# Kernel tuning notes

Measured on AMD Instinct MI355X. Metric: run time of the kernel, lower is better.

Reference implementation:

```python
import jax, jax.numpy as jnp
import numpy as np

D_MODEL = 1024
HIDDEN = 2048            # hidden_dimension // num_smaller_experts_per_expert
E_ROUTED = 14            # total_num_experts*num_smaller - num_shared
E_SHARED = 2
TOP_K = 2                # num_activated*num_smaller - num_shared
EPS = 1e-9               # config.epsilon
RMS_EPS = 1.1920929e-07  # torch RMSNorm default eps=None -> finfo(float32).eps


def setup_inputs() -> dict:
    key = jax.random.key(0)
    ks = jax.random.split(key, 9)
    B, T = 2, 1024
    x = jax.random.normal(ks[0], (B, T, D_MODEL), dtype=jnp.float32)
    router_w = jax.random.normal(ks[1], (D_MODEL, E_ROUTED), dtype=jnp.float32) * 0.006
    rms_w = jnp.ones((E_ROUTED, D_MODEL), dtype=jnp.float32)
    w1 = jax.random.normal(ks[2], (E_ROUTED, D_MODEL, HIDDEN), dtype=jnp.float32) * 0.02
    w2 = jax.random.normal(ks[3], (E_ROUTED, HIDDEN, D_MODEL), dtype=jnp.float32) * 0.02
    rms_w_s = jnp.ones((E_SHARED, D_MODEL), dtype=jnp.float32)
    w1_s = jax.random.normal(ks[4], (E_SHARED, D_MODEL, HIDDEN), dtype=jnp.float32) * 0.02
    w2_s = jax.random.normal(ks[5], (E_SHARED, HIDDEN, D_MODEL), dtype=jnp.float32) * 0.02
    return {"x": x, "router_w": router_w, "rms_w": rms_w, "w1": w1, "w2": w2,
            "rms_w_s": rms_w_s, "w1_s": w1_s, "w2_s": w2_s}


def _ffn(xn, rw, W1, W2):
    # RMSNorm -> Linear -> SiLU -> Linear (dropout is identity in eval)
    ms = jnp.mean(xn * xn, axis=-1, keepdims=True)
    h = (xn * jax.lax.rsqrt(ms + RMS_EPS)) * rw
    return jax.nn.silu(h @ W1) @ W2


def reference(x, router_w, rms_w, w1, w2, rms_w_s, w1_s, w2_s):
    B, T, D = x.shape
    N = B * T
    xf = x.reshape(N, D)
    # router gates + top-k sparsification + renormalization
    gates = jax.nn.softmax(xf @ router_w, axis=-1)          # [N, E]
    top_v, top_i = jax.lax.top_k(gates, TOP_K)              # [N, K]
    masked = jnp.zeros_like(gates).at[jnp.arange(N)[:, None], top_i].set(top_v)
    masked = masked / (masked.sum(axis=-1, keepdims=True) + EPS)  # [N, E]
    # routed experts: compute each expert on all tokens, combine with sparse gate weights
    # (same math as dispatch/index_add combine since masked is 0 off the top-k)
    routed = jax.vmap(lambda rw_, W1_, W2_: _ffn(xf, rw_, W1_, W2_))(rms_w, w1, w2)  # [E, N, D]
    routed_out = jnp.einsum('end,ne->nd', routed, masked)
    # shared experts: unweighted sum
    shared = jax.vmap(lambda rw_, W1_, W2_: _ffn(xf, rw_, W1_, W2_))(rms_w_s, w1_s, w2_s).sum(0)
    return (routed_out + shared).reshape(B, T, D)
```

## Files before the change

kernel.cpp:

```cpp
#include <hip/hip_runtime.h>
#include <hip/hip_bf16.h>
#include <cstdint>
#include <cstddef>

#define D_MODEL 1024
#define HIDDEN 2048
#define E_ROUTED 14
#define E_TOT 16
#define NTOK 2048
#define NASSIGN 4096
#define NROWS 8192

typedef __bf16 bf16x8 __attribute__((ext_vector_type(8)));
typedef float f32x4 __attribute__((ext_vector_type(4)));

static __device__ __forceinline__ unsigned short f2b(float f) {
  unsigned int u = __builtin_bit_cast(unsigned int, f);
  u += 0x7fffu + ((u >> 16) & 1u);
  return (unsigned short)(u >> 16);
}

#define ASYNC_COPY16(gptr, lptr)                                                        \
  __builtin_amdgcn_global_load_lds(                                                     \
      (const __attribute__((address_space(1))) unsigned int*)(gptr),                    \
      (__attribute__((address_space(3))) unsigned int*)(lptr), 16, 0, 0)

__global__ __launch_bounds__(256) void router_kernel(
    const float* __restrict__ x, const float* __restrict__ rweight,
    int* __restrict__ topi, float* __restrict__ topw,
    unsigned short* __restrict__ xhat) {
  int n = blockIdx.x, tid = threadIdx.x;
  const float4 xv = reinterpret_cast<const float4*>(x + (size_t)n * D_MODEL)[tid];
  float ss = xv.x * xv.x + xv.y * xv.y + xv.z * xv.z + xv.w * xv.w;
  float lg[E_ROUTED];
#pragma unroll
  for (int e = 0; e < E_ROUTED; ++e) lg[e] = 0.f;
  const float xa[4] = {xv.x, xv.y, xv.z, xv.w};
#pragma unroll
  for (int i = 0; i < 4; ++i) {
    const float* rw = rweight + (size_t)(tid * 4 + i) * E_ROUTED;
    float xd = xa[i];
#pragma unroll
    for (int e = 0; e < E_ROUTED; ++e) lg[e] = fmaf(xd, rw[e], lg[e]);
  }
#pragma unroll
  for (int off = 32; off > 0; off >>= 1) {
    ss += __shfl_xor(ss, off);
#pragma unroll
    for (int e = 0; e < E_ROUTED; ++e) lg[e] += __shfl_xor(lg[e], off);
  }
  __shared__ float red[4][16];
  int wid = tid >> 6, lane = tid & 63;
  if (lane == 0) {
    red[wid][0] = ss;
#pragma unroll
    for (int e = 0; e < E_ROUTED; ++e) red[wid][1 + e] = lg[e];
  }
  __syncthreads();
  __shared__ float s_scale;
  if (tid == 0) {
    float fin[15];
    for (int v = 0; v < 15; ++v) fin[v] = red[0][v] + red[1][v] + red[2][v] + red[3][v];
    s_scale = rsqrtf(fin[0] * (1.f / D_MODEL) + 1.1920929e-07f);
    float mx = fin[1];
    for (int e = 1; e < E_ROUTED; ++e) mx = fmaxf(mx, fin[1 + e]);
    float p[E_ROUTED]; float Z = 0.f;
    for (int e = 0; e < E_ROUTED; ++e) { p[e] = __expf(fin[1 + e] - mx); Z += p[e]; }
    int i0 = 0; float v0 = p[0];
    for (int e = 1; e < E_ROUTED; ++e) if (p[e] > v0) { v0 = p[e]; i0 = e; }
    int i1 = (i0 == 0) ? 1 : 0; float v1 = p[i1];
    for (int e = 0; e < E_ROUTED; ++e) if (e != i0 && p[e] > v1) { v1 = p[e]; i1 = e; }
    v0 /= Z; v1 /= Z;
    float inv = 1.f / (v0 + v1 + 1e-9f);
    topi[2 * n] = i0; topi[2 * n + 1] = i1;
    topw[2 * n] = v0 * inv; topw[2 * n + 1] = v1 * inv;
  }
  __syncthreads();
  float sc = s_scale;
  ushort4 hx;
  hx.x = f2b(xv.x * sc); hx.y = f2b(xv.y * sc);
  hx.z = f2b(xv.z * sc); hx.w = f2b(xv.w * sc);
  reinterpret_cast<ushort4*>(xhat + (size_t)n * D_MODEL)[tid] = hx;
}

__global__ __launch_bounds__(256) void count_kernel(const int* __restrict__ topi,
                                                    int* __restrict__ goff,
                                                    int* __restrict__ cursor) {
  __shared__ int cnt[E_ROUTED];
  int tid = threadIdx.x;
  if (tid < E_ROUTED) cnt[tid] = 0;
  __syncthreads();
  for (int i = tid; i < NASSIGN; i += 256) atomicAdd(&cnt[topi[i]], 1);
  __syncthreads();
  if (tid == 0) {
    int acc = 0;
    for (int e = 0; e < E_ROUTED; ++e) { goff[e] = acc; cursor[e] = acc; acc += cnt[e]; }
    goff[E_ROUTED] = acc;
  }
}

__global__ __launch_bounds__(256) void scatter_kernel(
    const int* __restrict__ topi, const float* __restrict__ topw,
    int* __restrict__ cursor, int* __restrict__ row_token,
    float* __restrict__ row_gate, int* __restrict__ token_rows) {
  int i = blockIdx.x * 256 + threadIdx.x;
  if (i >= NASSIGN) return;
  int e = topi[i];
  int pos = atomicAdd(&cursor[e], 1);
  row_token[pos] = i >> 1;
  row_gate[pos] = topw[i];
  token_rows[i] = pos;
}

template <int K, int N, bool SCALE>
__global__ __launch_bounds__(256) void convT_kernel(
    const float* __restrict__ Wr, const float* __restrict__ Ws,
    const float* __restrict__ RWr, const float* __restrict__ RWs,
    unsigned short* __restrict__ outT) {
  __shared__ float tile[64][65];
  int g = blockIdx.z;
  const float* src = (g < E_ROUTED) ? Wr + (size_t)g * K * N
                                    : Ws + (size_t)(g - E_ROUTED) * K * N;
  const float* rw = nullptr;
  if constexpr (SCALE)
    rw = (g < E_ROUTED) ? RWr + (size_t)g * K : RWs + (size_t)(g - E_ROUTED) * K;
  int k0 = blockIdx.y * 64, nn0 = blockIdx.x * 64;
  int t = threadIdx.x;
  int kk = t >> 4, nc = (t & 15) * 4;
#pragma unroll
  for (int j = 0; j < 4; ++j) {
    int k = kk + j * 16;
    float4 v = *(const float4*)(src + (size_t)(k0 + k) * N + nn0 + nc);
    float s = 1.f;
    if constexpr (SCALE) s = rw[k0 + k];
    tile[k][nc]     = v.x * s;
    tile[k][nc + 1] = v.y * s;
    tile[k][nc + 2] = v.z * s;
    tile[k][nc + 3] = v.w * s;
  }
  __syncthreads();
  int k8 = (t & 7) * 8;
#pragma unroll
  for (int p = 0; p < 2; ++p) {
    int n = (t >> 3) + p * 32;
    uint4 pk;
    pk.x = (unsigned)f2b(tile[k8 + 0][n]) | ((unsigned)f2b(tile[k8 + 1][n]) << 16);
    pk.y = (unsigned)f2b(tile[k8 + 2][n]) | ((unsigned)f2b(tile[k8 + 3][n]) << 16);
    pk.z = (unsigned)f2b(tile[k8 + 4][n]) | ((unsigned)f2b(tile[k8 + 5][n]) << 16);
    pk.w = (unsigned)f2b(tile[k8 + 6][n]) | ((unsigned)f2b(tile[k8 + 7][n]) << 16);
    *(uint4*)(outT + ((size_t)g * N + nn0 + n) * K + k0 + k8) = pk;
  }
}

template <bool G1, int KTOT, int NTOT>
__global__ __launch_bounds__(256, 3) void ffn_gemm(
    const int* __restrict__ goff, const int* __restrict__ row_token,
    const float* __restrict__ row_gate,
    const unsigned short* __restrict__ Abase,
    const unsigned short* __restrict__ Wt,
    unsigned short* __restrict__ Hout, float* __restrict__ Yout) {
  int g = blockIdx.z;
  int grpStart, cnt;
  if (g < E_ROUTED) { grpStart = goff[g]; cnt = goff[g + 1] - goff[g]; }
  else { grpStart = NASSIGN + (g - E_ROUTED) * NTOK; cnt = NTOK; }
  int m0 = blockIdx.y * 128;
  if (m0 >= cnt) return;
  int n0 = blockIdx.x * 128;

  __shared__ __align__(16) char smem[32 * 1024];
  char* sA = smem;
  char* sB = smem + 16 * 1024;

  int tid = threadIdx.x, lane = tid & 63, wid = tid >> 6;
  int wr = (wid >> 1) * 64, wc = (wid & 1) * 64;
  int lrow = lane >> 3;
  int swz = lrow << 4;
  int colB = ((lane & 7) << 4) ^ swz;

  const char* aSrc[4];
  const char* bSrc[4];
#pragma unroll
  for (int i = 0; i < 4; ++i) {
    int row = wid * 32 + i * 8 + lrow;
    int rIdx = m0 + row; if (rIdx >= cnt) rIdx = cnt - 1;
    int srcRow;
    if constexpr (G1) srcRow = (g < E_ROUTED) ? row_token[grpStart + rIdx] : rIdx;
    else srcRow = grpStart + rIdx;
    aSrc[i] = (const char*)(Abase + (size_t)srcRow * KTOT) + colB;
    bSrc[i] = (const char*)(Wt + ((size_t)g * NTOT + n0 + row) * KTOT) + colB;
  }

  f32x4 acc[4][4];
#pragma unroll
  for (int m = 0; m < 4; ++m)
#pragma unroll
    for (int n = 0; n < 4; ++n)
#pragma unroll
      for (int c = 0; c < 4; ++c) acc[m][n][c] = 0.f;

  for (int kt = 0; kt < KTOT / 64; ++kt) {
#pragma unroll
    for (int i = 0; i < 4; ++i) ASYNC_COPY16(aSrc[i], sA + wid * 4096 + i * 1024);
#pragma unroll
    for (int i = 0; i < 4; ++i) ASYNC_COPY16(bSrc[i], sB + wid * 4096 + i * 1024);
#pragma unroll
    for (int i = 0; i < 4; ++i) { aSrc[i] += 128; bSrc[i] += 128; }
    __syncthreads();

#pragma unroll
    for (int ks = 0; ks < 2; ++ks) {
      int kb = ks * 64 + ((lane >> 4) << 4);
      bf16x8 af[4], bfr[4];
#pragma unroll
      for (int m = 0; m < 4; ++m) {
        int r = wr + m * 16 + (lane & 15);
        af[m] = *(const bf16x8*)(sA + (r << 7) + (kb ^ ((r & 7) << 4)));
      }
#pragma unroll
      for (int n = 0; n < 4; ++n) {
        int r = wc + n * 16 + (lane & 15);
        bfr[n] = *(const bf16x8*)(sB + (r << 7) + (kb ^ ((r & 7) << 4)));
      }
#pragma unroll
      for (int m = 0; m < 4; ++m)
#pragma unroll
        for (int n = 0; n < 4; ++n)
          acc[m][n] = __builtin_amdgcn_mfma_f32_16x16x32_bf16(af[m], bfr[n], acc[m][n], 0, 0, 0);
    }
    __syncthreads();
  }

  int lr = (lane >> 4) * 4, lc = lane & 15;
#pragma unroll
  for (int m = 0; m < 4; ++m) {
    int rloc = m0 + wr + m * 16 + lr;
#pragma unroll
    for (int j = 0; j < 4; ++j) {
      if (rloc + j < cnt) {
        size_t r = (size_t)(grpStart + rloc + j);
        if constexpr (G1) {
#pragma unroll
          for (int n = 0; n < 4; ++n) {
            float v = acc[m][n][j];
            float sv = v / (1.f + __expf(-v));
            Hout[r * HIDDEN + (n0 + wc + n * 16 + lc)] = f2b(sv);
          }
        } else {
          float gate = 1.f;
          if (g < E_ROUTED) gate = row_gate[r];
#pragma unroll
          for (int n = 0; n < 4; ++n)
            Yout[r * D_MODEL + (n0 + wc + n * 16 + lc)] = acc[m][n][j] * gate;
        }
      }
    }
  }
}

__global__ __launch_bounds__(256) void combine_kernel(
    const float* __restrict__ y, const int* __restrict__ token_rows,
    float* __restrict__ out) {
  int n = blockIdx.x, tid = threadIdx.x;
  int a0 = token_rows[2 * n], a1 = token_rows[2 * n + 1];
  const float4* y0 = reinterpret_cast<const float4*>(y + (size_t)a0 * D_MODEL);
  const float4* y1 = reinterpret_cast<const float4*>(y + (size_t)a1 * D_MODEL);
  const float4* s0 = reinterpret_cast<const float4*>(y + (size_t)(NASSIGN + n) * D_MODEL);
  const float4* s1 = reinterpret_cast<const float4*>(y + (size_t)(NASSIGN + NTOK + n) * D_MODEL);
  float4 a = y0[tid], b = y1[tid], c = s0[tid], d = s1[tid];
  float4 r;
  r.x = a.x + b.x + c.x + d.x;
  r.y = a.y + b.y + c.y + d.y;
  r.z = a.z + b.z + c.z + d.z;
  r.w = a.w + b.w + c.w + d.w;
  reinterpret_cast<float4*>(out + (size_t)n * D_MODEL)[tid] = r;
}

extern "C" void kernel_launch(void* const* d_in, const int* in_sizes, int n_in,
                              void* d_out, int out_size, void* d_ws, size_t ws_size,
                              hipStream_t stream) {
  const float* x        = (const float*)d_in[0];
  const float* router_w = (const float*)d_in[1];
  const float* rms_w    = (const float*)d_in[2];
  const float* w1       = (const float*)d_in[3];
  const float* w2       = (const float*)d_in[4];
  const float* rms_w_s  = (const float*)d_in[5];
  const float* w1_s     = (const float*)d_in[6];
  const float* w2_s     = (const float*)d_in[7];
  float* out = (float*)d_out;

  char* ws = (char*)d_ws;
  unsigned short* xhat = (unsigned short*)ws;
  unsigned short* h    = (unsigned short*)(ws + ((size_t)4 << 20));
  float* y             = (float*)(ws + ((size_t)36 << 20));
  unsigned short* w1t  = (unsigned short*)(ws + ((size_t)68 << 20));
  unsigned short* w2t  = (unsigned short*)(ws + ((size_t)132 << 20));
  char* meta = ws + ((size_t)196 << 20);
  int*   topi       = (int*)(meta);
  float* topw       = (float*)(meta + (16 << 10));
  int*   row_token  = (int*)(meta + (32 << 10));
  float* row_gate   = (float*)(meta + (48 << 10));
  int*   token_rows = (int*)(meta + (64 << 10));
  int*   goff       = (int*)(meta + (80 << 10));
  int*   cursor     = (int*)(meta + (80 << 10) + 256);

  router_kernel<<<NTOK, 256, 0, stream>>>(x, router_w, topi, topw, xhat);
  count_kernel<<<1, 256, 0, stream>>>(topi, goff, cursor);
  scatter_kernel<<<NASSIGN / 256, 256, 0, stream>>>(topi, topw, cursor, row_token,
                                                    row_gate, token_rows);
  convT_kernel<D_MODEL, HIDDEN, true><<<dim3(HIDDEN / 64, D_MODEL / 64, E_TOT), 256, 0, stream>>>(
      w1, w1_s, rms_w, rms_w_s, w1t);
  convT_kernel<HIDDEN, D_MODEL, false><<<dim3(D_MODEL / 64, HIDDEN / 64, E_TOT), 256, 0, stream>>>(
      w2, w2_s, nullptr, nullptr, w2t);
  ffn_gemm<true, D_MODEL, HIDDEN><<<dim3(HIDDEN / 128, 16, E_TOT), 256, 0, stream>>>(
      goff, row_token, row_gate, xhat, w1t, h, nullptr);
  ffn_gemm<false, HIDDEN, D_MODEL><<<dim3(D_MODEL / 128, 16, E_TOT), 256, 0, stream>>>(
      goff, row_token, row_gate, h, w2t, nullptr, y);
  combine_kernel<<<NTOK, 256, 0, stream>>>(y, token_rows, out);
}
```

Baseline: 241.9 us.

## Merge weight transpose kernels and remap GEMM workgroups across XCDs

Merges the two weight convert/transpose launches into one kernel over a flat 16384-block grid, saving one launch and its tail. In the FFN GEMMs, the block index is remapped so consecutive tiles go to the same XCD (stride-8 interleave), aiming for better L2 reuse of weight and activation tiles. The remap makes early exit depend on the permuted row index, so blocks with no work are spread differently across the grid.

```diff
diff --git a/kernel.cpp b/kernel.cpp
--- a/kernel.cpp
+++ b/kernel.cpp
@@ -113,19 +113,10 @@
 }
 
 template <int K, int N, bool SCALE>
-__global__ __launch_bounds__(256) void convT_kernel(
-    const float* __restrict__ Wr, const float* __restrict__ Ws,
-    const float* __restrict__ RWr, const float* __restrict__ RWs,
-    unsigned short* __restrict__ outT) {
-  __shared__ float tile[64][65];
-  int g = blockIdx.z;
-  const float* src = (g < E_ROUTED) ? Wr + (size_t)g * K * N
-                                    : Ws + (size_t)(g - E_ROUTED) * K * N;
-  const float* rw = nullptr;
-  if constexpr (SCALE)
-    rw = (g < E_ROUTED) ? RWr + (size_t)g * K : RWs + (size_t)(g - E_ROUTED) * K;
-  int k0 = blockIdx.y * 64, nn0 = blockIdx.x * 64;
-  int t = threadIdx.x;
+static __device__ __forceinline__ void convT_body(
+    const float* __restrict__ src, const float* __restrict__ rw,
+    unsigned short* __restrict__ outT, float (*tile)[65],
+    int k0, int nn0, int t) {
   int kk = t >> 4, nc = (t & 15) * 4;
 #pragma unroll
   for (int j = 0; j < 4; ++j) {
@@ -148,7 +139,35 @@
     pk.y = (unsigned)f2b(tile[k8 + 2][n]) | ((unsigned)f2b(tile[k8 + 3][n]) << 16);
     pk.z = (unsigned)f2b(tile[k8 + 4][n]) | ((unsigned)f2b(tile[k8 + 5][n]) << 16);
     pk.w = (unsigned)f2b(tile[k8 + 6][n]) | ((unsigned)f2b(tile[k8 + 7][n]) << 16);
-    *(uint4*)(outT + ((size_t)g * N + nn0 + n) * K + k0 + k8) = pk;
+    *(uint4*)(outT + ((size_t)(nn0 + n)) * K + k0 + k8) = pk;
+  }
+}
+
+__global__ __launch_bounds__(256) void convT_both(
+    const float* __restrict__ w1, const float* __restrict__ w1_s,
+    const float* __restrict__ rms_w, const float* __restrict__ rms_w_s,
+    const float* __restrict__ w2, const float* __restrict__ w2_s,
+    unsigned short* __restrict__ w1t, unsigned short* __restrict__ w2t) {
+  __shared__ float tile[64][65];
+  int id = blockIdx.x, t = threadIdx.x;
+  constexpr int TPE1 = (HIDDEN / 64) * (D_MODEL / 64);
+  if (id < TPE1 * E_TOT) {
+    int g = id >> 9, tt = id & 511;
+    int nn0 = (tt & 31) * 64, k0 = (tt >> 5) * 64;
+    const float* src = (g < E_ROUTED) ? w1 + (size_t)g * D_MODEL * HIDDEN
+                                      : w1_s + (size_t)(g - E_ROUTED) * D_MODEL * HIDDEN;
+    const float* rw = (g < E_ROUTED) ? rms_w + (size_t)g * D_MODEL
+                                     : rms_w_s + (size_t)(g - E_ROUTED) * D_MODEL;
+    convT_body<D_MODEL, HIDDEN, true>(src, rw, w1t + (size_t)g * HIDDEN * D_MODEL,
+                                      tile, k0, nn0, t);
+  } else {
+    id -= TPE1 * E_TOT;
+    int g = id >> 9, tt = id & 511;
+    int nn0 = (tt & 15) * 64, k0 = (tt >> 4) * 64;
+    const float* src = (g < E_ROUTED) ? w2 + (size_t)g * HIDDEN * D_MODEL
+                                      : w2_s + (size_t)(g - E_ROUTED) * HIDDEN * D_MODEL;
+    convT_body<HIDDEN, D_MODEL, false>(src, nullptr, w2t + (size_t)g * D_MODEL * HIDDEN,
+                                       tile, k0, nn0, t);
   }
 }
 
@@ -163,94 +182,105 @@
   int grpStart, cnt;
   if (g < E_ROUTED) { grpStart = goff[g]; cnt = goff[g + 1] - goff[g]; }
   else { grpStart = NASSIGN + (g - E_ROUTED) * NTOK; cnt = NTOK; }
-  int m0 = blockIdx.y * 128;
-  if (m0 >= cnt) return;
-  int n0 = blockIdx.x * 128;
-
-  __shared__ __align__(16) char smem[32 * 1024];
-  char* sA = smem;
-  char* sB = smem + 16 * 1024;
-
-  int tid = threadIdx.x, lane = tid & 63, wid = tid >> 6;
-  int wr = (wid >> 1) * 64, wc = (wid & 1) * 64;
-  int lrow = lane >> 3;
-  int swz = lrow << 4;
-  int colB = ((lane & 7) << 4) ^ swz;
-
-  const char* aSrc[4];
-  const char* bSrc[4];
-#pragma unroll
-  for (int i = 0; i < 4; ++i) {
-    int row = wid * 32 + i * 8 + lrow;
-    int rIdx = m0 + row; if (rIdx >= cnt) rIdx = cnt - 1;
-    int srcRow;
-    if constexpr (G1) srcRow = (g < E_ROUTED) ? row_token[grpStart + rIdx] : rIdx;
-    else srcRow = grpStart + rIdx;
-    aSrc[i] = (const char*)(Abase + (size_t)srcRow * KTOT) + colB;
-    bSrc[i] = (const char*)(Wt + ((size_t)g * NTOT + n0 + row) * KTOT) + colB;
-  }
-
-  f32x4 acc[4][4];
-#pragma unroll
-  for (int m = 0; m < 4; ++m)
-#pragma unroll
-    for (int n = 0; n < 4; ++n)
-#pragma unroll
-      for (int c = 0; c < 4; ++c) acc[m][n][c] = 0.f;
-
-  for (int kt = 0; kt < KTOT / 64; ++kt) {
-#pragma unroll
-    for (int i = 0; i < 4; ++i) ASYNC_COPY16(aSrc[i], sA + wid * 4096 + i * 1024);
-#pragma unroll
-    for (int i = 0; i < 4; ++i) ASYNC_COPY16(bSrc[i], sB + wid * 4096 + i * 1024);
-#pragma unroll
-    for (int i = 0; i < 4; ++i) { aSrc[i] += 128; bSrc[i] += 128; }
-    __syncthreads();
-
-#pragma unroll
-    for (int ks = 0; ks < 2; ++ks) {
-      int kb = ks * 64 + ((lane >> 4) << 4);
-      bf16x8 af[4], bfr[4];
-#pragma unroll
-      for (int m = 0; m < 4; ++m) {
-        int r = wr + m * 16 + (lane & 15);
-        af[m] = *(const bf16x8*)(sA + (r << 7) + (kb ^ ((r & 7) << 4)));
+
+  {
+    int NX = gridDim.x, NY = gridDim.y;
+    int nwg = NX * NY;
+    int d = blockIdx.y * NX + blockIdx.x;
+    int cpx = nwg >> 3;
+    int w = (d & 7) * cpx + (d >> 3);
+    int myb = w % NY;
+    int nxb = w / NY;
+    if (myb * 128 >= cnt) return;
+    g = g;
+    int m0 = myb * 128;
+    int n0 = nxb * 128;
+
+    __shared__ __align__(16) char smem[32 * 1024];
+    char* sA = smem;
+    char* sB = smem + 16 * 1024;
+
+    int tid = threadIdx.x, lane = tid & 63, wid = tid >> 6;
+    int wr = (wid >> 1) * 64, wc = (wid & 1) * 64;
+    int lrow = lane >> 3;
+    int swz = lrow << 4;
+    int colB = ((lane & 7) << 4) ^ swz;
+
+    const char* aSrc[4];
+    const char* bSrc[4];
+#pragma unroll
+    for (int i = 0; i < 4; ++i) {
+      int row = wid * 32 + i * 8 + lrow;
+      int rIdx = m0 + row; if (rIdx >= cnt) rIdx = cnt - 1;
+      int srcRow;
+      if constexpr (G1) srcRow = (g < E_ROUTED) ? row_token[grpStart + rIdx] : rIdx;
+      else srcRow = grpStart + rIdx;
+      aSrc[i] = (const char*)(Abase + (size_t)srcRow * KTOT) + colB;
+      bSrc[i] = (const char*)(Wt + ((size_t)g * NTOT + n0 + row) * KTOT) + colB;
+    }
+
+    f32x4 acc[4][4];
+#pragma unroll
+    for (int m = 0; m < 4; ++m)
+#pragma unroll
+      for (int n = 0; n < 4; ++n)
+#pragma unroll
+        for (int c = 0; c < 4; ++c) acc[m][n][c] = 0.f;
+
+    for (int kt = 0; kt < KTOT / 64; ++kt) {
+#pragma unroll
+      for (int i = 0; i < 4; ++i) ASYNC_COPY16(aSrc[i], sA + wid * 4096 + i * 1024);
+#pragma unroll
+      for (int i = 0; i < 4; ++i) ASYNC_COPY16(bSrc[i], sB + wid * 4096 + i * 1024);
+#pragma unroll
+      for (int i = 0; i < 4; ++i) { aSrc[i] += 128; bSrc[i] += 128; }
+      __syncthreads();
+
+#pragma unroll
+      for (int ks = 0; ks < 2; ++ks) {
+        int kb = ks * 64 + ((lane >> 4) << 4);
+        bf16x8 af[4], bfr[4];
+#pragma unroll
+        for (int m = 0; m < 4; ++m) {
+          int r = wr + m * 16 + (lane & 15);
+          af[m] = *(const bf16x8*)(sA + (r << 7) + (kb ^ ((r & 7) << 4)));
+        }
+#pragma unroll
+        for (int n = 0; n < 4; ++n) {
+          int r = wc + n * 16 + (lane & 15);
+          bfr[n] = *(const bf16x8*)(sB + (r << 7) + (kb ^ ((r & 7) << 4)));
+        }
+#pragma unroll
+        for (int m = 0; m < 4; ++m)
+#pragma unroll
+          for (int n = 0; n < 4; ++n)
+            acc[m][n] = __builtin_amdgcn_mfma_f32_16x16x32_bf16(af[m], bfr[n], acc[m][n], 0, 0, 0);
       }
-#pragma unroll
-      for (int n = 0; n < 4; ++n) {
-        int r = wc + n * 16 + (lane & 15);
-        bfr[n] = *(const bf16x8*)(sB + (r << 7) + (kb ^ ((r & 7) << 4)));
-      }
-#pragma unroll
-      for (int m = 0; m < 4; ++m)
-#pragma unroll
-        for (int n = 0; n < 4; ++n)
-          acc[m][n] = __builtin_amdgcn_mfma_f32_16x16x32_bf16(af[m], bfr[n], acc[m][n], 0, 0, 0);
+      __syncthreads();
     }
-    __syncthreads();
-  }
-
-  int lr = (lane >> 4) * 4, lc = lane & 15;
-#pragma unroll
-  for (int m = 0; m < 4; ++m) {
-    int rloc = m0 + wr + m * 16 + lr;
-#pragma unroll
-    for (int j = 0; j < 4; ++j) {
-      if (rloc + j < cnt) {
-        size_t r = (size_t)(grpStart + rloc + j);
-        if constexpr (G1) {
-#pragma unroll
-          for (int n = 0; n < 4; ++n) {
-            float v = acc[m][n][j];
-            float sv = v / (1.f + __expf(-v));
-            Hout[r * HIDDEN + (n0 + wc + n * 16 + lc)] = f2b(sv);
+
+    int lr = (lane >> 4) * 4, lc = lane & 15;
+#pragma unroll
+    for (int m = 0; m < 4; ++m) {
+      int rloc = m0 + wr + m * 16 + lr;
+#pragma unroll
+      for (int j = 0; j < 4; ++j) {
+        if (rloc + j < cnt) {
+          size_t r = (size_t)(grpStart + rloc + j);
+          if constexpr (G1) {
+#pragma unroll
+            for (int n = 0; n < 4; ++n) {
+              float v = acc[m][n][j];
+              float sv = v / (1.f + __expf(-v));
+              Hout[r * HIDDEN + (n0 + wc + n * 16 + lc)] = f2b(sv);
+            }
+          } else {
+            float gate = 1.f;
+            if (g < E_ROUTED) gate = row_gate[r];
+#pragma unroll
+            for (int n = 0; n < 4; ++n)
+              Yout[r * D_MODEL + (n0 + wc + n * 16 + lc)] = acc[m][n][j] * gate;
           }
-        } else {
-          float gate = 1.f;
-          if (g < E_ROUTED) gate = row_gate[r];
-#pragma unroll
-          for (int n = 0; n < 4; ++n)
-            Yout[r * D_MODEL + (n0 + wc + n * 16 + lc)] = acc[m][n][j] * gate;
         }
       }
     }
@@ -284,8 +314,8 @@
   const float* w1       = (const float*)d_in[3];
   const float* w2       = (const float*)d_in[4];
   const float* rms_w_s  = (const float*)d_in[5];
-  const float* w1_s     = (const float*)d_in[6];
-  const float* w2_s     = (const float*)d_in[7];
+  const float* w1_s    = (const float*)d_in[6];
+  const float* w2_s    = (const float*)d_in[7];
   float* out = (float*)d_out;
 
   char* ws = (char*)d_ws;
@@ -307,10 +337,7 @@
   count_kernel<<<1, 256, 0, stream>>>(topi, goff, cursor);
   scatter_kernel<<<NASSIGN / 256, 256, 0, stream>>>(topi, topw, cursor, row_token,
                                                     row_gate, token_rows);
-  convT_kernel<D_MODEL, HIDDEN, true><<<dim3(HIDDEN / 64, D_MODEL / 64, E_TOT), 256, 0, stream>>>(
-      w1, w1_s, rms_w, rms_w_s, w1t);
-  convT_kernel<HIDDEN, D_MODEL, false><<<dim3(D_MODEL / 64, HIDDEN / 64, E_TOT), 256, 0, stream>>>(
-      w2, w2_s, nullptr, nullptr, w2t);
+  convT_both<<<16384, 256, 0, stream>>>(w1, w1_s, rms_w, rms_w_s, w2, w2_s, w1t, w2t);
   ffn_gemm<true, D_MODEL, HIDDEN><<<dim3(HIDDEN / 128, 16, E_TOT), 256, 0, stream>>>(
       goff, row_token, row_gate, xhat, w1t, h, nullptr);
   ffn_gemm<false, HIDDEN, D_MODEL><<<dim3(D_MODEL / 128, 16, E_TOT), 256, 0, stream>>>(
```

Result: no change. 242.2 us (+0.1%).

## Widen weight transpose tiles with bf16 LDS staging and remap GEMM blocks across XCDs

Applied to the files above, without the earlier changes.

The weight transpose-convert kernel now processes 64x256 tiles, converts to bf16 before staging in shared memory, and has each thread write a full 128-byte contiguous output row segment. This is meant to cut LDS traffic and improve write coalescing in the weight-prep pass, which moves large volumes of fp32 weights. Separately, the FFN GEMM remaps its block index so that blocks are distributed across the 8 XCDs, with neighbouring tiles on the same XCD to share L2. The remapping assumes the tile count is divisible by 8 and adds a little index arithmetic. The new LDS reads are 2-byte column reads with possible bank conflicts.

```diff
diff --git a/kernel.cpp b/kernel.cpp
--- a/kernel.cpp
+++ b/kernel.cpp
@@ -117,38 +117,38 @@
     const float* __restrict__ Wr, const float* __restrict__ Ws,
     const float* __restrict__ RWr, const float* __restrict__ RWs,
     unsigned short* __restrict__ outT) {
-  __shared__ float tile[64][65];
+  __shared__ unsigned short tile[64][256];
   int g = blockIdx.z;
   const float* src = (g < E_ROUTED) ? Wr + (size_t)g * K * N
                                     : Ws + (size_t)(g - E_ROUTED) * K * N;
   const float* rw = nullptr;
   if constexpr (SCALE)
     rw = (g < E_ROUTED) ? RWr + (size_t)g * K : RWs + (size_t)(g - E_ROUTED) * K;
-  int k0 = blockIdx.y * 64, nn0 = blockIdx.x * 64;
-  int t = threadIdx.x;
-  int kk = t >> 4, nc = (t & 15) * 4;
-#pragma unroll
-  for (int j = 0; j < 4; ++j) {
-    int k = kk + j * 16;
-    float4 v = *(const float4*)(src + (size_t)(k0 + k) * N + nn0 + nc);
+  int k0 = blockIdx.y * 64, n0 = blockIdx.x * 256;
+  int t = threadIdx.x, w = t >> 6, l = t & 63;
+
+#pragma unroll
+  for (int r = 0; r < 16; ++r) {
+    int row = r * 4 + w;
+    float4 v = *(const float4*)(src + (size_t)(k0 + row) * N + n0 + l * 4);
     float s = 1.f;
-    if constexpr (SCALE) s = rw[k0 + k];
-    tile[k][nc]     = v.x * s;
-    tile[k][nc + 1] = v.y * s;
-    tile[k][nc + 2] = v.z * s;
-    tile[k][nc + 3] = v.w * s;
-  }
-  __syncthreads();
-  int k8 = (t & 7) * 8;
-#pragma unroll
-  for (int p = 0; p < 2; ++p) {
-    int n = (t >> 3) + p * 32;
-    uint4 pk;
-    pk.x = (unsigned)f2b(tile[k8 + 0][n]) | ((unsigned)f2b(tile[k8 + 1][n]) << 16);
-    pk.y = (unsigned)f2b(tile[k8 + 2][n]) | ((unsigned)f2b(tile[k8 + 3][n]) << 16);
-    pk.z = (unsigned)f2b(tile[k8 + 4][n]) | ((unsigned)f2b(tile[k8 + 5][n]) << 16);
-    pk.w = (unsigned)f2b(tile[k8 + 6][n]) | ((unsigned)f2b(tile[k8 + 7][n]) << 16);
-    *(uint4*)(outT + ((size_t)g * N + nn0 + n) * K + k0 + k8) = pk;
+    if constexpr (SCALE) s = rw[k0 + row];
+    ushort4 b;
+    b.x = f2b(v.x * s); b.y = f2b(v.y * s);
+    b.z = f2b(v.z * s); b.w = f2b(v.w * s);
+    *(ushort4*)(&tile[row][l * 4]) = b;
+  }
+  __syncthreads();
+
+  unsigned short* dst = outT + ((size_t)g * N + n0 + t) * K + k0;
+#pragma unroll
+  for (int c = 0; c < 8; ++c) {
+    unsigned int u0 = (unsigned int)tile[c * 8 + 0][t] | ((unsigned int)tile[c * 8 + 1][t] << 16);
+    unsigned int u1 = (unsigned int)tile[c * 8 + 2][t] | ((unsigned int)tile[c * 8 + 3][t] << 16);
+    unsigned int u2 = (unsigned int)tile[c * 8 + 4][t] | ((unsigned int)tile[c * 8 + 5][t] << 16);
+    unsigned int u3 = (unsigned int)tile[c * 8 + 6][t] | ((unsigned int)tile[c * 8 + 7][t] << 16);
+    uint4 pk = {u0, u1, u2, u3};
+    *(uint4*)(dst + c * 8) = pk;
   }
 }
 
@@ -163,94 +163,104 @@
   int grpStart, cnt;
   if (g < E_ROUTED) { grpStart = goff[g]; cnt = goff[g + 1] - goff[g]; }
   else { grpStart = NASSIGN + (g - E_ROUTED) * NTOK; cnt = NTOK; }
-  int m0 = blockIdx.y * 128;
-  if (m0 >= cnt) return;
-  int n0 = blockIdx.x * 128;
-
-  __shared__ __align__(16) char smem[32 * 1024];
-  char* sA = smem;
-  char* sB = smem + 16 * 1024;
-
-  int tid = threadIdx.x, lane = tid & 63, wid = tid >> 6;
-  int wr = (wid >> 1) * 64, wc = (wid & 1) * 64;
-  int lrow = lane >> 3;
-  int swz = lrow << 4;
-  int colB = ((lane & 7) << 4) ^ swz;
-
-  const char* aSrc[4];
-  const char* bSrc[4];
-#pragma unroll
-  for (int i = 0; i < 4; ++i) {
-    int row = wid * 32 + i * 8 + lrow;
-    int rIdx = m0 + row; if (rIdx >= cnt) rIdx = cnt - 1;
-    int srcRow;
-    if constexpr (G1) srcRow = (g < E_ROUTED) ? row_token[grpStart + rIdx] : rIdx;
-    else srcRow = grpStart + rIdx;
-    aSrc[i] = (const char*)(Abase + (size_t)srcRow * KTOT) + colB;
-    bSrc[i] = (const char*)(Wt + ((size_t)g * NTOT + n0 + row) * KTOT) + colB;
-  }
-
-  f32x4 acc[4][4];
-#pragma unroll
-  for (int m = 0; m < 4; ++m)
-#pragma unroll
-    for (int n = 0; n < 4; ++n)
-#pragma unroll
-      for (int c = 0; c < 4; ++c) acc[m][n][c] = 0.f;
-
-  for (int kt = 0; kt < KTOT / 64; ++kt) {
-#pragma unroll
-    for (int i = 0; i < 4; ++i) ASYNC_COPY16(aSrc[i], sA + wid * 4096 + i * 1024);
-#pragma unroll
-    for (int i = 0; i < 4; ++i) ASYNC_COPY16(bSrc[i], sB + wid * 4096 + i * 1024);
-#pragma unroll
-    for (int i = 0; i < 4; ++i) { aSrc[i] += 128; bSrc[i] += 128; }
-    __syncthreads();
-
-#pragma unroll
-    for (int ks = 0; ks < 2; ++ks) {
-      int kb = ks * 64 + ((lane >> 4) << 4);
-      bf16x8 af[4], bfr[4];
-#pragma unroll
-      for (int m = 0; m < 4; ++m) {
-        int r = wr + m * 16 + (lane & 15);
-        af[m] = *(const bf16x8*)(sA + (r << 7) + (kb ^ ((r & 7) << 4)));
+
+  {
+    int NX = gridDim.x, NY = gridDim.y;
+    int nwg = NX * NY;
+    int d = blockIdx.y * NX + blockIdx.x;
+    int cpx = nwg >> 3;
+    int w = (d & 7) * cpx + (d >> 3);
+    int myb = w % NY;
+    int nxb = w / NY;
+    if (myb * 128 >= cnt) return;
+    int m0 = myb * 128;
+    int n0 = nxb * 128;
+
+    __shared__ __align__(16) char smem[32 * 1024];
+    char* sA = smem;
+    char* sB = smem + 16 * 1024;
+
+    int tid = threadIdx.x, lane = tid & 63, wid = tid >> 6;
+    int wr = (wid >> 1) * 64, wc = (wid & 1) * 64;
+    int lrow = lane >> 3;
+    int swz = lrow << 4;
+    int colB = ((lane & 7) << 4) ^ swz;
+
+    const char* aSrc[4];
+    const char* bSrc[4];
+#pragma unroll
+    for (int i = 0; i < 4; ++i) {
+      int row = wid * 32 + i * 8 + lrow;
+      int rIdx = m0 + row; if (rIdx >= cnt) rIdx = cnt - 1;
+      int srcRow;
+      if constexpr (G1) srcRow = (g < E_ROUTED) ? row_token[grpStart + rIdx] : rIdx;
+      else srcRow = grpStart + rIdx;
+      aSrc[i] = (const char*)(Abase + (size_t)srcRow * KTOT) + colB;
+      bSrc[i] = (const char*)(Wt + ((size_t)g * NTOT + n0 + row) * KTOT) + colB;
+    }
+
+    f32x4 acc[4][4];
+#pragma unroll
+    for (int m = 0; m < 4; ++m)
+#pragma unroll
+      for (int n = 0; n < 4; ++n)
+#pragma unroll
+        for (int c = 0; c < 4; ++c) acc[m][n][c] = 0.f;
+
+    for (int kt = 0; kt < KTOT / 64; ++kt) {
+#pragma unroll
+      for (int i = 0; i < 4; ++i) ASYNC_COPY16(aSrc[i], sA + wid * 4096 + i * 1024);
+#pragma unroll
+      for (int i = 0; i < 4; ++i) ASYNC_COPY16(bSrc[i], sB + wid * 4096 + i * 1024);
+#pragma unroll
+      for (int i = 0; i < 4; ++i) { aSrc[i] += 128; bSrc[i] += 128; }
+      __syncthreads();
+
+#pragma unroll
+      for (int ks = 0; ks < 2; ++ks) {
+        int kb = ks * 64 + ((lane >> 4) << 4);
+        bf16x8 af[4], bfr[4];
+#pragma unroll
+        for (int m = 0; m < 4; ++m) {
+          int r = wr + m * 16 + (lane & 15);
+          af[m] = *(const bf16x8*)(sA + (r << 7) + (kb ^ ((r & 7) << 4)));
+        }
+#pragma unroll
+        for (int n = 0; n < 4; ++n) {
+          int r = wc + n * 16 + (lane & 15);
+          bfr[n] = *(const bf16x8*)(sB + (r << 7) + (kb ^ ((r & 7) << 4)));
+        }
+#pragma unroll
+        for (int m = 0; m < 4; ++m)
+#pragma unroll
+          for (int n = 0; n < 4; ++n)
+            acc[m][n] = __builtin_amdgcn_mfma_f32_16x16x32_bf16(af[m], bfr[n], acc[m][n], 0, 0, 0);
       }
-#pragma unroll
-      for (int n = 0; n < 4; ++n) {
-        int r = wc + n * 16 + (lane & 15);
-        bfr[n] = *(const bf16x8*)(sB + (r << 7) + (kb ^ ((r & 7) << 4)));
-      }
-#pragma unroll
-      for (int m = 0; m < 4; ++m)
-#pragma unroll
-        for (int n = 0; n < 4; ++n)
-          acc[m][n] = __builtin_amdgcn_mfma_f32_16x16x32_bf16(af[m], bfr[n], acc[m][n], 0, 0, 0);
+      __syncthreads();
     }
-    __syncthreads();
-  }
-
-  int lr = (lane >> 4) * 4, lc = lane & 15;
-#pragma unroll
-  for (int m = 0; m < 4; ++m) {
-    int rloc = m0 + wr + m * 16 + lr;
-#pragma unroll
-    for (int j = 0; j < 4; ++j) {
-      if (rloc + j < cnt) {
-        size_t r = (size_t)(grpStart + rloc + j);
-        if constexpr (G1) {
-#pragma unroll
-          for (int n = 0; n < 4; ++n) {
-            float v = acc[m][n][j];
-            float sv = v / (1.f + __expf(-v));
-            Hout[r * HIDDEN + (n0 + wc + n * 16 + lc)] = f2b(sv);
+
+    int lr = (lane >> 4) * 4, lc = lane & 15;
+#pragma unroll
+    for (int m = 0; m < 4; ++m) {
+      int rloc = m0 + wr + m * 16 + lr;
+#pragma unroll
+      for (int j = 0; j < 4; ++j) {
+        if (rloc + j < cnt) {
+          size_t r = (size_t)(grpStart + rloc + j);
+          if constexpr (G1) {
+#pragma unroll
+            for (int n = 0; n < 4; ++n) {
+              float v = acc[m][n][j];
+              float sv = v / (1.f + __expf(-v));
+              Hout[r * HIDDEN + (n0 + wc + n * 16 + lc)] = f2b(sv);
+            }
+          } else {
+            float gate = 1.f;
+            if (g < E_ROUTED) gate = row_gate[r];
+#pragma unroll
+            for (int n = 0; n < 4; ++n)
+              Yout[r * D_MODEL + (n0 + wc + n * 16 + lc)] = acc[m][n][j] * gate;
           }
-        } else {
-          float gate = 1.f;
-          if (g < E_ROUTED) gate = row_gate[r];
-#pragma unroll
-          for (int n = 0; n < 4; ++n)
-            Yout[r * D_MODEL + (n0 + wc + n * 16 + lc)] = acc[m][n][j] * gate;
         }
       }
     }
@@ -284,8 +294,8 @@
   const float* w1       = (const float*)d_in[3];
   const float* w2       = (const float*)d_in[4];
   const float* rms_w_s  = (const float*)d_in[5];
-  const float* w1_s     = (const float*)d_in[6];
-  const float* w2_s     = (const float*)d_in[7];
+  const float* w1_s    = (const float*)d_in[6];
+  const float* w2_s    = (const float*)d_in[7];
   float* out = (float*)d_out;
 
   char* ws = (char*)d_ws;
@@ -307,9 +317,9 @@
   count_kernel<<<1, 256, 0, stream>>>(topi, goff, cursor);
   scatter_kernel<<<NASSIGN / 256, 256, 0, stream>>>(topi, topw, cursor, row_token,
                                                     row_gate, token_rows);
-  convT_kernel<D_MODEL, HIDDEN, true><<<dim3(HIDDEN / 64, D_MODEL / 64, E_TOT), 256, 0, stream>>>(
+  convT_kernel<D_MODEL, HIDDEN, true><<<dim3(HIDDEN / 256, D_MODEL / 64, E_TOT), 256, 0, stream>>>(
       w1, w1_s, rms_w, rms_w_s, w1t);
-  convT_kernel<HIDDEN, D_MODEL, false><<<dim3(D_MODEL / 64, HIDDEN / 64, E_TOT), 256, 0, stream>>>(
+  convT_kernel<HIDDEN, D_MODEL, false><<<dim3(D_MODEL / 256, HIDDEN / 64, E_TOT), 256, 0, stream>>>(
       w2, w2_s, nullptr, nullptr, w2t);
   ffn_gemm<true, D_MODEL, HIDDEN><<<dim3(HIDDEN / 128, 16, E_TOT), 256, 0, stream>>>(
       goff, row_token, row_gate, xhat, w1t, h, nullptr);
```

Result: slower. 273.1 us (+12.9%).

## Make grouped FFN GEMMs persistent with a compact tile list and XCD-chunked scheduling

Applied to the files above, without the earlier changes.

The count kernel now builds prefix sums of tile counts per expert group. Both FFN GEMMs then launch a fixed grid of 768 persistent workgroups that walk a compact list of real tiles instead of a 3D grid full of early-exiting blocks. Each XCD (blockIdx&7) takes a contiguous range of tiles, ordered M-fastest within an expert, so weight tiles are shared in that XCD's L2. This removes empty-block launch overhead and improves cache locality, at the cost of a linear group search per tile and possible tail imbalance across XCDs.

```diff
diff --git a/kernel.cpp b/kernel.cpp
--- a/kernel.cpp
+++ b/kernel.cpp
@@ -10,6 +10,7 @@
 #define NTOK 2048
 #define NASSIGN 4096
 #define NROWS 8192
+#define GEMM_NWG 768
 
 typedef __bf16 bf16x8 __attribute__((ext_vector_type(8)));
 typedef float f32x4 __attribute__((ext_vector_type(4)));
@@ -85,7 +86,9 @@
 
 __global__ __launch_bounds__(256) void count_kernel(const int* __restrict__ topi,
                                                     int* __restrict__ goff,
-                                                    int* __restrict__ cursor) {
+                                                    int* __restrict__ cursor,
+                                                    int* __restrict__ base1,
+                                                    int* __restrict__ base2) {
   __shared__ int cnt[E_ROUTED];
   int tid = threadIdx.x;
   if (tid < E_ROUTED) cnt[tid] = 0;
@@ -96,6 +99,15 @@
     int acc = 0;
     for (int e = 0; e < E_ROUTED; ++e) { goff[e] = acc; cursor[e] = acc; acc += cnt[e]; }
     goff[E_ROUTED] = acc;
+    int b1 = 0, b2 = 0;
+    for (int g = 0; g < E_TOT; ++g) {
+      base1[g] = b1; base2[g] = b2;
+      int c = (g < E_ROUTED) ? cnt[g] : NTOK;
+      int mt = (c + 127) >> 7;
+      b1 += mt * (HIDDEN / 128);
+      b2 += mt * (D_MODEL / 128);
+    }
+    base1[E_TOT] = b1; base2[E_TOT] = b2;
   }
 }
 
@@ -154,103 +166,120 @@
 
 template <bool G1, int KTOT, int NTOT>
 __global__ __launch_bounds__(256, 3) void ffn_gemm(
-    const int* __restrict__ goff, const int* __restrict__ row_token,
-    const float* __restrict__ row_gate,
+    const int* __restrict__ goff, const int* __restrict__ base,
+    const int* __restrict__ row_token, const float* __restrict__ row_gate,
     const unsigned short* __restrict__ Abase,
     const unsigned short* __restrict__ Wt,
     unsigned short* __restrict__ Hout, float* __restrict__ Yout) {
-  int g = blockIdx.z;
-  int grpStart, cnt;
-  if (g < E_ROUTED) { grpStart = goff[g]; cnt = goff[g + 1] - goff[g]; }
-  else { grpStart = NASSIGN + (g - E_ROUTED) * NTOK; cnt = NTOK; }
-  int m0 = blockIdx.y * 128;
-  if (m0 >= cnt) return;
-  int n0 = blockIdx.x * 128;
-
   __shared__ __align__(16) char smem[32 * 1024];
-  char* sA = smem;
-  char* sB = smem + 16 * 1024;
+  __shared__ int sbase[E_TOT + 1];
+  __shared__ int sgoff[E_ROUTED + 1];
 
   int tid = threadIdx.x, lane = tid & 63, wid = tid >> 6;
+  if (tid <= E_TOT) sbase[tid] = base[tid];
+  if (tid >= 32 && tid <= 32 + E_ROUTED) sgoff[tid - 32] = goff[tid - 32];
+  __syncthreads();
+
+  int xcd = blockIdx.x & 7, slot = blockIdx.x >> 3;
+  int total = sbase[E_TOT];
+  int chunk = (total + 7) >> 3;
+  int cend = min((xcd + 1) * chunk, total);
+
   int wr = (wid >> 1) * 64, wc = (wid & 1) * 64;
   int lrow = lane >> 3;
   int swz = lrow << 4;
   int colB = ((lane & 7) << 4) ^ swz;
-
-  const char* aSrc[4];
-  const char* bSrc[4];
-#pragma unroll
-  for (int i = 0; i < 4; ++i) {
-    int row = wid * 32 + i * 8 + lrow;
-    int rIdx = m0 + row; if (rIdx >= cnt) rIdx = cnt - 1;
-    int srcRow;
-    if constexpr (G1) srcRow = (g < E_ROUTED) ? row_token[grpStart + rIdx] : rIdx;
-    else srcRow = grpStart + rIdx;
-    aSrc[i] = (const char*)(Abase + (size_t)srcRow * KTOT) + colB;
-    bSrc[i] = (const char*)(Wt + ((size_t)g * NTOT + n0 + row) * KTOT) + colB;
-  }
-
-  f32x4 acc[4][4];
-#pragma unroll
-  for (int m = 0; m < 4; ++m)
-#pragma unroll
-    for (int n = 0; n < 4; ++n)
-#pragma unroll
-      for (int c = 0; c < 4; ++c) acc[m][n][c] = 0.f;
-
-  for (int kt = 0; kt < KTOT / 64; ++kt) {
-#pragma unroll
-    for (int i = 0; i < 4; ++i) ASYNC_COPY16(aSrc[i], sA + wid * 4096 + i * 1024);
-#pragma unroll
-    for (int i = 0; i < 4; ++i) ASYNC_COPY16(bSrc[i], sB + wid * 4096 + i * 1024);
-#pragma unroll
-    for (int i = 0; i < 4; ++i) { aSrc[i] += 128; bSrc[i] += 128; }
-    __syncthreads();
-
-#pragma unroll
-    for (int ks = 0; ks < 2; ++ks) {
-      int kb = ks * 64 + ((lane >> 4) << 4);
-      bf16x8 af[4], bfr[4];
-#pragma unroll
-      for (int m = 0; m < 4; ++m) {
-        int r = wr + m * 16 + (lane & 15);
-        af[m] = *(const bf16x8*)(sA + (r << 7) + (kb ^ ((r & 7) << 4)));
+  int l15 = lane & 15;
+
+  for (int c = xcd * chunk + slot; c < cend; c += (GEMM_NWG >> 3)) {
+    int g = 0;
+    while (sbase[g + 1] <= c) ++g;
+    int grpStart, cnt;
+    if (g < E_ROUTED) { grpStart = sgoff[g]; cnt = sgoff[g + 1] - sgoff[g]; }
+    else { grpStart = NASSIGN + (g - E_ROUTED) * NTOK; cnt = NTOK; }
+    int mtg = (cnt + 127) >> 7;
+    int r = c - sbase[g];
+    int nxb = r / mtg;
+    int myb = r - nxb * mtg;
+    int m0 = myb * 128, n0 = nxb * 128;
+
+    char* sA = smem;
+    char* sB = smem + 16 * 1024;
+    const char* aSrc[4];
+    const char* bSrc[4];
+#pragma unroll
+    for (int i = 0; i < 4; ++i) {
+      int row = wid * 32 + i * 8 + lrow;
+      int rIdx = m0 + row; if (rIdx >= cnt) rIdx = cnt - 1;
+      int srcRow;
+      if constexpr (G1) srcRow = (g < E_ROUTED) ? row_token[grpStart + rIdx] : rIdx;
+      else srcRow = grpStart + rIdx;
+      aSrc[i] = (const char*)(Abase + (size_t)srcRow * KTOT) + colB;
+      bSrc[i] = (const char*)(Wt + ((size_t)g * NTOT + n0 + row) * KTOT) + colB;
+    }
+
+    f32x4 acc[4][4];
+#pragma unroll
+    for (int m = 0; m < 4; ++m)
+#pragma unroll
+      for (int n = 0; n < 4; ++n)
+#pragma unroll
+        for (int cc = 0; cc < 4; ++cc) acc[m][n][cc] = 0.f;
+
+    for (int kt = 0; kt < KTOT / 64; ++kt) {
+#pragma unroll
+      for (int i = 0; i < 4; ++i) ASYNC_COPY16(aSrc[i], sA + wid * 4096 + i * 1024);
+#pragma unroll
+      for (int i = 0; i < 4; ++i) ASYNC_COPY16(bSrc[i], sB + wid * 4096 + i * 1024);
+#pragma unroll
+      for (int i = 0; i < 4; ++i) { aSrc[i] += 128; bSrc[i] += 128; }
+      __syncthreads();
+
+#pragma unroll
+      for (int ks = 0; ks < 2; ++ks) {
+        int kb = ks * 64 + ((lane >> 4) << 4);
+        bf16x8 af[4], bfr[4];
+#pragma unroll
+        for (int m = 0; m < 4; ++m) {
+          int rr = wr + m * 16 + l15;
+          af[m] = *(const bf16x8*)(sA + (rr << 7) + (kb ^ ((rr & 7) << 4)));
+        }
+#pragma unroll
+        for (int n = 0; n < 4; ++n) {
+          int rr = wc + n * 16 + l15;
+          bfr[n] = *(const bf16x8*)(sB + (rr << 7) + (kb ^ ((rr & 7) << 4)));
+        }
+#pragma unroll
+        for (int m = 0; m < 4; ++m)
+#pragma unroll
+          for (int n = 0; n < 4; ++n)
+            acc[m][n] = __builtin_amdgcn_mfma_f32_16x16x32_bf16(af[m], bfr[n], acc[m][n], 0, 0, 0);
       }
-#pragma unroll
-      for (int n = 0; n < 4; ++n) {
-        int r = wc + n * 16 + (lane & 15);
-        bfr[n] = *(const bf16x8*)(sB + (r << 7) + (kb ^ ((r & 7) << 4)));
-      }
-#pragma unroll
-      for (int m = 0; m < 4; ++m)
-#pragma unroll
-        for (int n = 0; n < 4; ++n)
-          acc[m][n] = __builtin_amdgcn_mfma_f32_16x16x32_bf16(af[m], bfr[n], acc[m][n], 0, 0, 0);
+      __syncthreads();
     }
-    __syncthreads();
-  }
-
-  int lr = (lane >> 4) * 4, lc = lane & 15;
-#pragma unroll
-  for (int m = 0; m < 4; ++m) {
-    int rloc = m0 + wr + m * 16 + lr;
-#pragma unroll
-    for (int j = 0; j < 4; ++j) {
-      if (rloc + j < cnt) {
-        size_t r = (size_t)(grpStart + rloc + j);
-        if constexpr (G1) {
-#pragma unroll
-          for (int n = 0; n < 4; ++n) {
-            float v = acc[m][n][j];
-            float sv = v / (1.f + __expf(-v));
-            Hout[r * HIDDEN + (n0 + wc + n * 16 + lc)] = f2b(sv);
+
+    int lr = (lane >> 4) * 4;
+#pragma unroll
+    for (int m = 0; m < 4; ++m) {
+      int rloc = m0 + wr + m * 16 + lr;
+#pragma unroll
+      for (int j = 0; j < 4; ++j) {
+        if (rloc + j < cnt) {
+          size_t rg = (size_t)(grpStart + rloc + j);
+          if constexpr (G1) {
+#pragma unroll
+            for (int n = 0; n < 4; ++n) {
+              float v = acc[m][n][j];
+              float sv = v / (1.f + __expf(-v));
+              Hout[rg * HIDDEN + (n0 + wc + n * 16 + l15)] = f2b(sv);
+            }
+          } else {
+            float gate = 1.f;
+            if (g < E_ROUTED) gate = row_gate[rg];
+#pragma unroll
+            for (int n = 0; n < 4; ++n)
+              Yout[rg * D_MODEL + (n0 + wc + n * 16 + l15)] = acc[m][n][j] * gate;
           }
-        } else {
-          float gate = 1.f;
-          if (g < E_ROUTED) gate = row_gate[r];
-#pragma unroll
-          for (int n = 0; n < 4; ++n)
-            Yout[r * D_MODEL + (n0 + wc + n * 16 + lc)] = acc[m][n][j] * gate;
         }
       }
     }
@@ -284,8 +313,8 @@
   const float* w1       = (const float*)d_in[3];
   const float* w2       = (const float*)d_in[4];
   const float* rms_w_s  = (const float*)d_in[5];
-  const float* w1_s     = (const float*)d_in[6];
-  const float* w2_s     = (const float*)d_in[7];
+  const float* w1_s    = (const float*)d_in[6];
+  const float* w2_s    = (const float*)d_in[7];
   float* out = (float*)d_out;
 
   char* ws = (char*)d_ws;
@@ -301,19 +330,21 @@
   float* row_gate   = (float*)(meta + (48 << 10));
   int*   token_rows = (int*)(meta + (64 << 10));
   int*   goff       = (int*)(meta + (80 << 10));
-  int*   cursor     = (int*)(meta + (80 << 10) + 256);
+  int*   cursor     = (int*)(meta + (80 << 10) + 128);
+  int*   base1      = (int*)(meta + (80 << 10) + 256);
+  int*   base2      = (int*)(meta + (80 << 10) + 384);
 
   router_kernel<<<NTOK, 256, 0, stream>>>(x, router_w, topi, topw, xhat);
-  count_kernel<<<1, 256, 0, stream>>>(topi, goff, cursor);
+  count_kernel<<<1, 256, 0, stream>>>(topi, goff, cursor, base1, base2);
   scatter_kernel<<<NASSIGN / 256, 256, 0, stream>>>(topi, topw, cursor, row_token,
                                                     row_gate, token_rows);
   convT_kernel<D_MODEL, HIDDEN, true><<<dim3(HIDDEN / 64, D_MODEL / 64, E_TOT), 256, 0, stream>>>(
       w1, w1_s, rms_w, rms_w_s, w1t);
   convT_kernel<HIDDEN, D_MODEL, false><<<dim3(D_MODEL / 64, HIDDEN / 64, E_TOT), 256, 0, stream>>>(
       w2, w2_s, nullptr, nullptr, w2t);
-  ffn_gemm<true, D_MODEL, HIDDEN><<<dim3(HIDDEN / 128, 16, E_TOT), 256, 0, stream>>>(
-      goff, row_token, row_gate, xhat, w1t, h, nullptr);
-  ffn_gemm<false, HIDDEN, D_MODEL><<<dim3(D_MODEL / 128, 16, E_TOT), 256, 0, stream>>>(
-      goff, row_token, row_gate, h, w2t, nullptr, y);
+  ffn_gemm<true, D_MODEL, HIDDEN><<<GEMM_NWG, 256, 0, stream>>>(
+      goff, base1, row_token, row_gate, xhat, w1t, h, nullptr);
+  ffn_gemm<false, HIDDEN, D_MODEL><<<GEMM_NWG, 256, 0, stream>>>(
+      goff, base2, row_token, row_gate, h, w2t, nullptr, y);
   combine_kernel<<<NTOK, 256, 0, stream>>>(y, token_rows, out);
 }
```

Result: faster. 232.8 us, median of 2 (-3.8%).
